# Performance work log

Measured on AMD Instinct MI355X. Metric: run time of the kernel, lower is better.

## Reference

```python
import jax, jax.numpy as jnp
import numpy as np

B, F, E, H, D = 8192, 40, 128, 4, 4
DH = E // H  # per-head attention dim
STD = 0.05   # all params init N(0, 0.05) in the torch module (including LayerNorm!)


def setup_inputs() -> dict:
    key = jax.random.key(0)
    ks = jax.random.split(key, 7)
    inputs = jax.random.normal(ks[0], (B, F, E), dtype=jnp.float32)
    # domain ids in [1, D] so every row belongs to some domain (torch masks domain_ids == i+1)
    domain_ids = jax.random.randint(ks[1], (B,), 1, D + 1)
    W_Queries = jax.random.normal(ks[2], (D, E, E), dtype=jnp.float32) * STD  # domain_W_Queries
    W_Value = jax.random.normal(ks[3], (E, E), dtype=jnp.float32) * STD
    W_Res = jax.random.normal(ks[4], (E, E), dtype=jnp.float32) * STD
    ln_gamma = jax.random.normal(ks[5], (D, E), dtype=jnp.float32) * STD  # per-domain LayerNorm weight
    ln_beta = jax.random.normal(ks[6], (D, E), dtype=jnp.float32) * STD   # per-domain LayerNorm bias
    return dict(inputs=inputs, domain_ids=domain_ids, W_Queries=W_Queries,
                W_Value=W_Value, W_Res=W_Res, ln_gamma=ln_gamma, ln_beta=ln_beta)


def reference(inputs, domain_ids, W_Queries, W_Value, W_Res, ln_gamma, ln_beta):
    d = domain_ids - 1  # (B,) zero-based domain index
    # value projection is shared across domains
    v = jnp.einsum('bfe,eh->bfh', inputs, W_Value).reshape(B, F, H, DH)
    # merge='no': the key projection is domain_W_Queries[0] for EVERY domain (source quirk)
    k = jnp.einsum('bfe,eh->bfh', inputs, W_Queries[0]).reshape(B, F, H, DH)
    # per-sample domain-routed query projection
    Wq_b = W_Queries[d]  # (B, E, E) gather
    q = jnp.einsum('bfe,beh->bfh', inputs, Wq_b).reshape(B, F, H, DH)
    # scaled multi-head attention over the field axis (F x F per head)
    scores = jnp.einsum('bihd,bjhd->bhij', q, k) / np.float32(np.sqrt(DH))
    attn = jax.nn.softmax(scores, axis=-1)  # attn_dropout is identity in eval mode
    out = jnp.einsum('bhij,bjhd->bihd', attn, v).reshape(B, F, E)
    # residual projection + relu
    out = jax.nn.relu(out + jnp.einsum('bfe,eh->bfh', inputs, W_Res))
    # per-domain LayerNorm (eps=1e-6), params gathered per sample
    mean = out.mean(axis=-1, keepdims=True)
    var = ((out - mean) ** 2).mean(axis=-1, keepdims=True)
    normed = (out - mean) / jnp.sqrt(var + 1e-6)
    return normed * ln_gamma[d][:, None, :] + ln_beta[d][:, None, :]
```

## Files before the change

### kernel.cpp

```cpp
#include <hip/hip_runtime.h>
#include <hip/hip_bf16.h>

typedef __attribute__((ext_vector_type(4))) float f32x4;
typedef __attribute__((ext_vector_type(8))) short s16x8;
typedef unsigned long long u64;

namespace {
constexpr int B_   = 8192;
constexpr int NT   = 256;
constexpr int SPB  = 8;
constexpr int NBLK = B_ / SPB;
constexpr int XS_SH = 48 * 136;
constexpr int REDF  = 48 * 4 * 2;
constexpr int OSTR  = 132;
constexpr int OSTF  = 40 * OSTR;
constexpr int RED_B = 2 * XS_SH * 2;
constexpr int OUT_B = RED_B + 2 * REDF * 4;
constexpr int POOL_B = OUT_B + 2 * OSTF * 4;
}

__device__ __forceinline__ ushort f2b(float f) {
    union { __hip_bfloat16 h; ushort u; } cv;
    cv.h = __float2bfloat16(f);
    return cv.u;
}
__device__ __forceinline__ unsigned bfpair(float x, float y) {
    const unsigned ux = __float_as_uint(x) + 0x8000u;
    const unsigned uy = __float_as_uint(y) + 0x8000u;
    return (ux >> 16) | (uy & 0xFFFF0000u);
}
__device__ __forceinline__ u64 pack4(f32x4 v) {
    return (u64)bfpair(v[0], v[1]) | ((u64)bfpair(v[2], v[3]) << 32);
}
__device__ __forceinline__ u64 pack4f(float4 v) {
    return (u64)bfpair(v.x, v.y) | ((u64)bfpair(v.z, v.w) << 32);
}
__device__ __forceinline__ s16x8 cat(u64 A, u64 B) {
    union { u64 q[2]; s16x8 v; } r;
    r.q[0] = A; r.q[1] = B;
    return r.v;
}
#define MFMA(a, b, c) __builtin_amdgcn_mfma_f32_16x16x32_bf16((a), (b), (c), 0, 0, 0)

__global__ void convert_w(const float* __restrict__ Wq,
                          const float* __restrict__ Wv,
                          const float* __restrict__ Wr,
                          ushort* __restrict__ Wt)
{
    int idx = blockIdx.x * 256 + threadIdx.x;
    if (idx >= 6 * 16384) return;
    int m = idx >> 14, r = idx & 16383, n = r >> 7, k = r & 127;
    float v;
    if (m < 4)       v = Wq[(size_t)m * 16384 + k * 128 + n];
    else if (m == 4) v = Wv[k * 128 + n];
    else             v = Wr[k * 128 + n];
    Wt[idx] = f2b(v);
}

__global__ __launch_bounds__(NT, 2)
void mdr_fused14(const float* __restrict__ inputs,
                 const int* __restrict__ dom,
                 const ushort* __restrict__ Wt,
                 const float* __restrict__ ln_g,
                 const float* __restrict__ ln_b,
                 float* __restrict__ out)
{
    __shared__ __align__(16) char pool[POOL_B];
    ushort* sp  = reinterpret_cast<ushort*>(pool);
    float* red  = reinterpret_cast<float*>(pool + RED_B);
    float* ost  = reinterpret_cast<float*>(pool + OUT_B);

    const int t = threadIdx.x;
    const int w = t >> 6, l = t & 63;
    const int lr = l & 15, lc = l >> 4;
    const int h = w;
    const size_t s0 = (size_t)blockIdx.x * SPB;
    const float4* in4 = reinterpret_cast<const float4*>(inputs);
    float4* out4g = reinterpret_cast<float4*>(out);

    {
        const int row = 40 + (t >> 5), c = (t & 31) * 4;
        *reinterpret_cast<u64*>(&sp[row * 136 + c]) = 0ull;
        *reinterpret_cast<u64*>(&sp[XS_SH + row * 136 + c]) = 0ull;
    }

    float4 xp[5];
    #pragma unroll
    for (int j = 0; j < 5; ++j)
        xp[j] = in4[s0 * 1280 + t + 256 * j];
    #pragma unroll
    for (int j = 0; j < 5; ++j) {
        const int idx4 = t + 256 * j;
        const int row = idx4 >> 5, c4 = idx4 & 31;
        *reinterpret_cast<u64*>(&sp[row * 136 + c4 * 4]) = pack4f(xp[j]);
    }
    __syncthreads();

    #pragma unroll 1
    for (int s = 0; s < SPB; ++s) {
        const int b = s & 1;
        ushort* xs  = sp + b * XS_SH;
        float* redb = red + b * REDF;
        float* ostb = ost + b * OSTF;
        const int d = dom[s0 + s] - 1;

        const ushort* wq = Wt + (size_t)d * 16384 + (h * 32) * 128;
        const ushort* wk = Wt + (h * 32) * 128;
        const ushort* wv = Wt + (size_t)4 * 16384 + (h * 32) * 128;
        const ushort* wr = Wt + (size_t)5 * 16384 + (h * 32) * 128;
        const int wo = lr * 128 + lc * 8;

        f32x4 aq[2][3], ak[2][3];
        #pragma unroll
        for (int nt = 0; nt < 2; ++nt)
            #pragma unroll
            for (int rt = 0; rt < 3; ++rt) {
                aq[nt][rt] = f32x4{0.f, 0.f, 0.f, 0.f};
                ak[nt][rt] = f32x4{0.f, 0.f, 0.f, 0.f};
            }
        #pragma unroll
        for (int kk = 0; kk < 4; ++kk) {
            s16x8 xf[3];
            #pragma unroll
            for (int rt = 0; rt < 3; ++rt)
                xf[rt] = *reinterpret_cast<const s16x8*>(&xs[(rt * 16 + lr) * 136 + kk * 32 + lc * 8]);
            #pragma unroll
            for (int nt = 0; nt < 2; ++nt) {
                const int o = nt * 2048 + wo + kk * 32;
                const s16x8 qf = *reinterpret_cast<const s16x8*>(wq + o);
                const s16x8 kf = *reinterpret_cast<const s16x8*>(wk + o);
                #pragma unroll
                for (int rt = 0; rt < 3; ++rt) {
                    aq[nt][rt] = MFMA(qf, xf[rt], aq[nt][rt]);
                    ak[nt][rt] = MFMA(kf, xf[rt], ak[nt][rt]);
                }
            }
        }
        s16x8 qfr[3], kfr[3];
        #pragma unroll
        for (int tt = 0; tt < 3; ++tt) {
            qfr[tt] = cat(pack4(aq[0][tt]), pack4(aq[1][tt]));
            kfr[tt] = cat(pack4(ak[0][tt]), pack4(ak[1][tt]));
        }

        f32x4 av[3][2], ar[2][3];
        #pragma unroll
        for (int nt = 0; nt < 2; ++nt)
            #pragma unroll
            for (int rt = 0; rt < 3; ++rt) {
                av[rt][nt] = f32x4{0.f, 0.f, 0.f, 0.f};
                ar[nt][rt] = f32x4{0.f, 0.f, 0.f, 0.f};
            }
        #pragma unroll
        for (int kk = 0; kk < 4; ++kk) {
            s16x8 xf[3];
            #pragma unroll
            for (int rt = 0; rt < 3; ++rt)
                xf[rt] = *reinterpret_cast<const s16x8*>(&xs[(rt * 16 + lr) * 136 + kk * 32 + lc * 8]);
            #pragma unroll
            for (int nt = 0; nt < 2; ++nt) {
                const int o = nt * 2048 + wo + kk * 32;
                const s16x8 vf = *reinterpret_cast<const s16x8*>(wv + o);
                const s16x8 rf = *reinterpret_cast<const s16x8*>(wr + o);
                #pragma unroll
                for (int rt = 0; rt < 3; ++rt) {
                    av[rt][nt] = MFMA(xf[rt], vf, av[rt][nt]);
                    ar[nt][rt] = MFMA(rf, xf[rt], ar[nt][rt]);
                }
            }
        }
        u64 pkV[3][2];
        #pragma unroll
        for (int rt = 0; rt < 3; ++rt)
            #pragma unroll
            for (int nt = 0; nt < 2; ++nt)
                pkV[rt][nt] = pack4(av[rt][nt]);

        const float scale = 0.17677669529663689f;
        u64 pkP[3][3];
        float inv[3];
        #pragma unroll
        for (int it = 0; it < 3; ++it) {
            f32x4 sr[3];
            #pragma unroll
            for (int jt = 0; jt < 3; ++jt) {
                f32x4 z = {0.f, 0.f, 0.f, 0.f};
                sr[jt] = MFMA(kfr[jt], qfr[it], z);
            }
            float sum = 0.f;
            #pragma unroll
            for (int jt = 0; jt < 3; ++jt) {
                f32x4 pv;
                #pragma unroll
                for (int reg = 0; reg < 4; ++reg) {
                    float p = (jt == 2 && lc >= 2) ? 0.f : __expf(sr[jt][reg] * scale);
                    pv[reg] = p;
                    sum += p;
                }
                pkP[it][jt] = pack4(pv);
            }
            sum += __shfl_xor(sum, 16);
            sum += __shfl_xor(sum, 32);
            inv[it] = 1.f / sum;
        }

        if (s + 1 < SPB) {
            #pragma unroll
            for (int j = 0; j < 5; ++j)
                xp[j] = in4[(s0 + s + 1) * 1280 + t + 256 * j];
        }

        f32x4 o[2][3];
        #pragma unroll
        for (int et = 0; et < 2; ++et)
            #pragma unroll
            for (int it = 0; it < 3; ++it)
                o[et][it] = f32x4{0.f, 0.f, 0.f, 0.f};
        #pragma unroll
        for (int kk = 0; kk < 2; ++kk) {
            s16x8 vfr[2], pfr[3];
            #pragma unroll
            for (int et = 0; et < 2; ++et)
                vfr[et] = kk ? cat(pkV[2][et], 0ull)
                             : cat(pkV[0][et], pkV[1][et]);
            #pragma unroll
            for (int it = 0; it < 3; ++it)
                pfr[it] = kk ? cat(pkP[it][2], 0ull)
                             : cat(pkP[it][0], pkP[it][1]);
            #pragma unroll
            for (int et = 0; et < 2; ++et)
                #pragma unroll
                for (int it = 0; it < 3; ++it)
                    o[et][it] = MFMA(vfr[et], pfr[it], o[et][it]);
        }

        #pragma unroll
        for (int it = 0; it < 3; ++it) {
            const bool valid = !(it == 2 && lr >= 8);
            float sa = 0.f, qa2 = 0.f;
            float4 yv[2];
            #pragma unroll
            for (int et = 0; et < 2; ++et)
                #pragma unroll
                for (int reg = 0; reg < 4; ++reg) {
                    float yy = fmaxf(fmaf(o[et][it][reg], inv[it], ar[et][it][reg]), 0.f);
                    (&yv[et].x)[reg] = yy;
                    sa += yy;
                    qa2 = fmaf(yy, yy, qa2);
                }
            sa  += __shfl_xor(sa, 16);   sa  += __shfl_xor(sa, 32);
            qa2 += __shfl_xor(qa2, 16);  qa2 += __shfl_xor(qa2, 32);
            if (lc == 0)
                *reinterpret_cast<float2*>(&redb[((it * 16 + lr) * 4 + w) * 2]) =
                    make_float2(sa, qa2);
            if (valid) {
                #pragma unroll
                for (int et = 0; et < 2; ++et)
                    *reinterpret_cast<float4*>(&ostb[(it * 16 + lr) * OSTR + h * 32 + et * 16 + 4 * lc]) = yv[et];
            }
        }

        if (s + 1 < SPB) {
            ushort* xsn = sp + ((s + 1) & 1) * XS_SH;
            #pragma unroll
            for (int j = 0; j < 5; ++j) {
                const int idx4 = t + 256 * j;
                const int row = idx4 >> 5, c4 = idx4 & 31;
                *reinterpret_cast<u64*>(&xsn[row * 136 + c4 * 4]) = pack4f(xp[j]);
            }
        }
        __syncthreads();

        const int c4r = t & 31;
        const float4 gvr = *reinterpret_cast<const float4*>(&ln_g[d * 128 + c4r * 4]);
        const float4 bvr = *reinterpret_cast<const float4*>(&ln_b[d * 128 + c4r * 4]);
        const size_t b4 = (s0 + s) * 1280;
        #pragma unroll
        for (int j5 = 0; j5 < 5; ++j5) {
            const int idx = j5 * 256 + t;
            const int row = idx >> 5;
            const float4 r01 = *reinterpret_cast<const float4*>(&redb[row * 8]);
            const float4 r23 = *reinterpret_cast<const float4*>(&redb[row * 8 + 4]);
            const float sa = r01.x + r01.z + r23.x + r23.z;
            const float q2 = r01.y + r01.w + r23.y + r23.w;
            const float mean = sa * (1.f / 128.f);
            const float rstd = rsqrtf(q2 * (1.f / 128.f) - mean * mean + 1e-6f);
            const float4 v = *reinterpret_cast<const float4*>(&ostb[row * OSTR + c4r * 4]);
            float4 ov;
            ov.x = (v.x - mean) * rstd * gvr.x + bvr.x;
            ov.y = (v.y - mean) * rstd * gvr.y + bvr.y;
            ov.z = (v.z - mean) * rstd * gvr.z + bvr.z;
            ov.w = (v.w - mean) * rstd * gvr.w + bvr.w;
            out4g[b4 + idx] = ov;
        }
    }
}

extern "C" void kernel_launch(void* const* d_in, const int* in_sizes, int n_in,
                              void* d_out, int out_size, void* d_ws, size_t ws_size,
                              hipStream_t stream)
{
    const float* inputs = (const float*)d_in[0];
    const int*   dm     = (const int*)d_in[1];
    const float* Wq     = (const float*)d_in[2];
    const float* Wv     = (const float*)d_in[3];
    const float* Wr     = (const float*)d_in[4];
    const float* g      = (const float*)d_in[5];
    const float* bt     = (const float*)d_in[6];
    float* outp         = (float*)d_out;
    ushort* Wt          = (ushort*)d_ws;

    convert_w<<<(6 * 16384 + 255) / 256, 256, 0, stream>>>(Wq, Wv, Wr, Wt);
    mdr_fused14<<<NBLK, NT, 0, stream>>>(inputs, dm, Wt, g, bt, outp);
}
```

Measured before the change: 159.7 us.

## Defer LayerNorm epilogue to next iteration and issue input prefetch earlier

Moves the per-sample LayerNorm/output store of sample s-1 into iteration s after the single barrier, so its global stores overlap with the next sample's MFMA work. The shared-memory staging of the input is moved to the top of each iteration, and the next-sample global prefetch is issued earlier, before the softmax. This adds a tail epilogue after the loop and raises register pressure from holding the prefetch longer.

```diff
diff --git a/kernel.cpp b/kernel.cpp
--- a/kernel.cpp
+++ b/kernel.cpp
@@ -58,7 +58,7 @@
 }
 
 __global__ __launch_bounds__(NT, 2)
-void mdr_fused14(const float* __restrict__ inputs,
+void mdr_fused15(const float* __restrict__ inputs,
                  const int* __restrict__ dom,
                  const ushort* __restrict__ Wt,
                  const float* __restrict__ ln_g,
@@ -77,6 +77,7 @@
     const size_t s0 = (size_t)blockIdx.x * SPB;
     const float4* in4 = reinterpret_cast<const float4*>(inputs);
     float4* out4g = reinterpret_cast<float4*>(out);
+    const int c4r = t & 31;
 
     {
         const int row = 40 + (t >> 5), c = (t & 31) * 4;
@@ -88,13 +89,7 @@
     #pragma unroll
     for (int j = 0; j < 5; ++j)
         xp[j] = in4[s0 * 1280 + t + 256 * j];
-    #pragma unroll
-    for (int j = 0; j < 5; ++j) {
-        const int idx4 = t + 256 * j;
-        const int row = idx4 >> 5, c4 = idx4 & 31;
-        *reinterpret_cast<u64*>(&sp[row * 136 + c4 * 4]) = pack4f(xp[j]);
-    }
-    __syncthreads();
+    int pd = 0;
 
     #pragma unroll 1
     for (int s = 0; s < SPB; ++s) {
@@ -102,7 +97,41 @@
         ushort* xs  = sp + b * XS_SH;
         float* redb = red + b * REDF;
         float* ostb = ost + b * OSTF;
+
+        #pragma unroll
+        for (int j = 0; j < 5; ++j) {
+            const int idx4 = t + 256 * j;
+            const int row = idx4 >> 5, c4 = idx4 & 31;
+            *reinterpret_cast<u64*>(&xs[row * 136 + c4 * 4]) = pack4f(xp[j]);
+        }
         const int d = dom[s0 + s] - 1;
+        __syncthreads();
+
+        if (s > 0) {
+            const float* redp = red + (b ^ 1) * REDF;
+            const float* ostp = ost + (b ^ 1) * OSTF;
+            const float4 gvr = *reinterpret_cast<const float4*>(&ln_g[pd * 128 + c4r * 4]);
+            const float4 bvr = *reinterpret_cast<const float4*>(&ln_b[pd * 128 + c4r * 4]);
+            const size_t b4 = (s0 + s - 1) * 1280;
+            #pragma unroll
+            for (int j5 = 0; j5 < 5; ++j5) {
+                const int idx = j5 * 256 + t;
+                const int row = idx >> 5;
+                const float4 r01 = *reinterpret_cast<const float4*>(&redp[row * 8]);
+                const float4 r23 = *reinterpret_cast<const float4*>(&redp[row * 8 + 4]);
+                const float sa = r01.x + r01.z + r23.x + r23.z;
+                const float q2 = r01.y + r01.w + r23.y + r23.w;
+                const float mean = sa * (1.f / 128.f);
+                const float rstd = rsqrtf(q2 * (1.f / 128.f) - mean * mean + 1e-6f);
+                const float4 v = *reinterpret_cast<const float4*>(&ostp[row * OSTR + c4r * 4]);
+                float4 ov;
+                ov.x = (v.x - mean) * rstd * gvr.x + bvr.x;
+                ov.y = (v.y - mean) * rstd * gvr.y + bvr.y;
+                ov.z = (v.z - mean) * rstd * gvr.z + bvr.z;
+                ov.w = (v.w - mean) * rstd * gvr.w + bvr.w;
+                out4g[b4 + idx] = ov;
+            }
+        }
 
         const ushort* wq = Wt + (size_t)d * 16384 + (h * 32) * 128;
         const ushort* wk = Wt + (h * 32) * 128;
@@ -175,6 +204,12 @@
             #pragma unroll
             for (int nt = 0; nt < 2; ++nt)
                 pkV[rt][nt] = pack4(av[rt][nt]);
+
+        if (s + 1 < SPB) {
+            #pragma unroll
+            for (int j = 0; j < 5; ++j)
+                xp[j] = in4[(s0 + s + 1) * 1280 + t + 256 * j];
+        }
 
         const float scale = 0.17677669529663689f;
         u64 pkP[3][3];
@@ -202,12 +237,6 @@
             sum += __shfl_xor(sum, 16);
             sum += __shfl_xor(sum, 32);
             inv[it] = 1.f / sum;
-        }
-
-        if (s + 1 < SPB) {
-            #pragma unroll
-            for (int j = 0; j < 5; ++j)
-                xp[j] = in4[(s0 + s + 1) * 1280 + t + 256 * j];
         }
 
         f32x4 o[2][3];
@@ -259,33 +288,28 @@
                     *reinterpret_cast<float4*>(&ostb[(it * 16 + lr) * OSTR + h * 32 + et * 16 + 4 * lc]) = yv[et];
             }
         }
-
-        if (s + 1 < SPB) {
-            ushort* xsn = sp + ((s + 1) & 1) * XS_SH;
-            #pragma unroll
-            for (int j = 0; j < 5; ++j) {
-                const int idx4 = t + 256 * j;
-                const int row = idx4 >> 5, c4 = idx4 & 31;
-                *reinterpret_cast<u64*>(&xsn[row * 136 + c4 * 4]) = pack4f(xp[j]);
-            }
-        }
-        __syncthreads();
-
-        const int c4r = t & 31;
-        const float4 gvr = *reinterpret_cast<const float4*>(&ln_g[d * 128 + c4r * 4]);
-        const float4 bvr = *reinterpret_cast<const float4*>(&ln_b[d * 128 + c4r * 4]);
-        const size_t b4 = (s0 + s) * 1280;
+        pd = d;
+    }
+
+    __syncthreads();
+    {
+        const int b = (SPB - 1) & 1;
+        const float* redp = red + b * REDF;
+        const float* ostp = ost + b * OSTF;
+        const float4 gvr = *reinterpret_cast<const float4*>(&ln_g[pd * 128 + c4r * 4]);
+        const float4 bvr = *reinterpret_cast<const float4*>(&ln_b[pd * 128 + c4r * 4]);
+        const size_t b4 = (s0 + SPB - 1) * 1280;
         #pragma unroll
         for (int j5 = 0; j5 < 5; ++j5) {
             const int idx = j5 * 256 + t;
             const int row = idx >> 5;
-            const float4 r01 = *reinterpret_cast<const float4*>(&redb[row * 8]);
-            const float4 r23 = *reinterpret_cast<const float4*>(&redb[row * 8 + 4]);
+            const float4 r01 = *reinterpret_cast<const float4*>(&redp[row * 8]);
+            const float4 r23 = *reinterpret_cast<const float4*>(&redp[row * 8 + 4]);
             const float sa = r01.x + r01.z + r23.x + r23.z;
             const float q2 = r01.y + r01.w + r23.y + r23.w;
             const float mean = sa * (1.f / 128.f);
             const float rstd = rsqrtf(q2 * (1.f / 128.f) - mean * mean + 1e-6f);
-            const float4 v = *reinterpret_cast<const float4*>(&ostb[row * OSTR + c4r * 4]);
+            const float4 v = *reinterpret_cast<const float4*>(&ostp[row * OSTR + c4r * 4]);
             float4 ov;
             ov.x = (v.x - mean) * rstd * gvr.x + bvr.x;
             ov.y = (v.y - mean) * rstd * gvr.y + bvr.y;
@@ -311,5 +335,5 @@
     ushort* Wt          = (ushort*)d_ws;
 
     convert_w<<<(6 * 16384 + 255) / 256, 256, 0, stream>>>(Wq, Wv, Wr, Wt);
-    mdr_fused14<<<NBLK, NT, 0, stream>>>(inputs, dm, Wt, g, bt, outp);
-}
+    mdr_fused15<<<NBLK, NT, 0, stream>>>(inputs, dm, Wt, g, bt, outp);
+}
```

Result: slower. 192.4 us (+20.5%).
